# Performance work log

Hardware: AMD Instinct MI355X
Metric: run time of the kernel (lower is better)

Reference implementation:

```python
import jax, jax.numpy as jnp
import numpy as np

BUCKET_SIZE = 128
CAUSAL = True
LOOK_BACKWARD = 1
LOOK_FORWARD = 0


def look_around(x, backward=LOOK_BACKWARD, forward=LOOK_FORWARD, pad_value=-1.0):
    # x: [n, buckets, bucket_size, ...]; pad along bucket dim, gather halo windows along dim 2
    nb = x.shape[1]
    pad = [(0, 0), (backward, forward)] + [(0, 0)] * (x.ndim - 2)
    p = jnp.pad(x, pad, constant_values=pad_value)
    return jnp.concatenate([p[:, i:i + nb] for i in range(forward + backward + 1)], axis=2)


def setup_inputs() -> dict:
    key = jax.random.key(0)
    kq, kk, kv = jax.random.split(key, 3)
    shape = (4, 16, 8192, 64)  # [batch, heads, seq, head_dim]
    return {
        "q": jax.random.normal(kq, shape, jnp.float32),
        "k": jax.random.normal(kk, shape, jnp.float32),
        "v": jax.random.normal(kv, shape, jnp.float32),
    }


def reference(q, k, v):
    b, h, t, e = q.shape
    buckets = t // BUCKET_SIZE
    ticker = jnp.arange(t, dtype=q.dtype).reshape(1, buckets, BUCKET_SIZE)

    def bkt(x):
        return x.reshape(b * h, buckets, BUCKET_SIZE, e)

    bq, bk, bv = bkt(q), bkt(k), bkt(v)
    bk = look_around(bk)
    bv = look_around(bv)
    bq_t = ticker                # [1, buckets, bucket_size]
    bq_k = look_around(ticker)

    dots = jnp.einsum('nbie,nbje->nbij', bq, bk) * (e ** -0.5)
    mask_value = -jnp.finfo(dots.dtype).max
    if CAUSAL:
        causal_mask = bq_t[:, :, :, None] < bq_k[:, :, None, :]
        dots = jnp.where(causal_mask, mask_value, dots)
    pad_mask = bq_k[:, :, None, :] == -1
    dots = jnp.where(pad_mask, mask_value, dots)

    attn = jax.nn.softmax(dots, axis=-1)
    out = jnp.einsum('nbij,nbje->nbie', attn, bv)
    return out.reshape(b, h, t, e)
```

## Files before the change

### kernel.cpp

```cpp
#include <hip/hip_runtime.h>
#include <hip/hip_bf16.h>

#define T_SEQ 8192
#define E 64
#define BS 128
#define QSCALE 0.18033688f

typedef __attribute__((ext_vector_type(4))) float f32x4;
typedef __attribute__((ext_vector_type(8))) short bf16x8;

__device__ __forceinline__ float hw_exp2(float x) {
    float r;
    asm("v_exp_f32 %0, %1" : "=v"(r) : "v"(x));
    return r;
}

__device__ __forceinline__ unsigned pk2(float a, float b) {
    __hip_bfloat162 h = __float22bfloat162_rn(make_float2(a, b));
    union { __hip_bfloat162 h; unsigned u; } cv; cv.h = h;
    return cv.u;
}

union Frag { unsigned u[4]; bf16x8 v; };

__global__ __launch_bounds__(256, 2)
void la_kernel(const float* __restrict__ q, const float* __restrict__ k,
               const float* __restrict__ v, float* __restrict__ out) {
    __shared__ __align__(16) unsigned char smem[32768];
    unsigned short* KV = (unsigned short*)smem;
    float* OB = (float*)smem;

    const int raw  = blockIdx.x;
    const int work = (raw & 7) * 512 + (raw >> 3);
    const int bh = work >> 6;
    const int qb = work & 63;

    const int tid  = threadIdx.x;
    const int wv   = tid >> 6;
    const int lane = tid & 63;
    const int g    = lane >> 4;
    const int col  = lane & 15;

    const size_t base_kv = (size_t)bh * T_SEQ * E;
    const int k0 = (qb - 1) * BS;
    const int STT = (qb == 0) ? 8 : 0;
    const int SKT = (qb == 0) ? 4 : 0;

    bf16x8 qf0[2], qf1[2];
    #pragma unroll
    for (int it = 0; it < 2; ++it) {
        #pragma unroll
        for (int kq = 0; kq < 2; ++kq) {
            const float* src = q + ((size_t)bh * T_SEQ + qb * BS + wv * 32 + it * 16 + col) * E
                                 + g * 8 + kq * 32;
            float4 f0 = *(const float4*)(src);
            float4 f1 = *(const float4*)(src + 4);
            Frag fr;
            fr.u[0] = pk2(f0.x * QSCALE, f0.y * QSCALE);
            fr.u[1] = pk2(f0.z * QSCALE, f0.w * QSCALE);
            fr.u[2] = pk2(f1.x * QSCALE, f1.y * QSCALE);
            fr.u[3] = pk2(f1.z * QSCALE, f1.w * QSCALE);
            if (it) qf1[kq] = fr.v; else qf0[kq] = fr.v;
        }
    }

    {
        const int jr = tid >> 4;
        const int c4 = (tid & 15) * 4;
        #pragma unroll
        for (int t = 0; t < 16; ++t) {
            const int jj = jr + t * 16;
            const int gk = k0 + jj;
            float4 kvv = make_float4(0.f, 0.f, 0.f, 0.f);
            if (gk >= 0) kvv = *(const float4*)(k + base_kv + (size_t)gk * E + c4);
            uint2 pr;
            pr.x = pk2(kvv.x, kvv.y);
            pr.y = pk2(kvv.z, kvv.w);
            *(uint2*)(&KV[(jj * 64 + c4) ^ ((jj & 7) << 3)]) = pr;
        }
    }
    __syncthreads();

    unsigned P0[32], P1[32];
    float inv0, inv1;

    auto s_phase = [&](const int it, const bf16x8* qf, unsigned* __restrict__ P, float& inv_out) {
        const int NT = 2 * wv + it + 9;
        f32x4 S[16];
        #pragma unroll
        for (int jt = 0; jt < 16; ++jt) S[jt] = (f32x4)0.f;
        #pragma unroll
        for (int jt = 0; jt < 16; ++jt) {
            if (jt >= STT && jt < NT) {
                const int j = jt * 16 + col;
                #pragma unroll
                for (int kq = 0; kq < 2; ++kq) {
                    const int e = g * 8 + kq * 32;
                    bf16x8 kf = *(const bf16x8*)(&KV[(j * 64 + e) ^ ((j & 7) << 3)]);
                    S[jt] = __builtin_amdgcn_mfma_f32_16x16x32_bf16(kf, qf[kq], S[jt], 0, 0, 0);
                }
            }
        }
        float mx = -3.0e38f;
        #pragma unroll
        for (int jt = 0; jt < 16; ++jt) {
            if (jt >= STT && jt < NT) {
                if (jt == NT - 1) {
                    #pragma unroll
                    for (int r = 0; r < 4; ++r) {
                        float s = (4 * g + r <= col) ? S[jt][r] : -1.0e30f;
                        S[jt][r] = s;
                        mx = fmaxf(mx, s);
                    }
                } else {
                    #pragma unroll
                    for (int r = 0; r < 4; ++r) mx = fmaxf(mx, S[jt][r]);
                }
            }
        }
        mx = fmaxf(mx, __shfl_xor(mx, 16, 64));
        mx = fmaxf(mx, __shfl_xor(mx, 32, 64));
        float sum = 0.f;
        #pragma unroll
        for (int jt = 0; jt < 16; ++jt) {
            if (jt >= STT && jt < NT) {
                #pragma unroll
                for (int r = 0; r < 4; ++r) {
                    float p = hw_exp2(S[jt][r] - mx);
                    S[jt][r] = p;
                    sum += p;
                }
            }
        }
        sum += __shfl_xor(sum, 16, 64);
        sum += __shfl_xor(sum, 32, 64);
        inv_out = 1.0f / sum;
        const int NKT = wv + 5;
        #pragma unroll
        for (int kt = 0; kt < 8; ++kt) {
            if (kt >= SKT && kt < NKT) {
                P[4*kt+0] = pk2(S[2*kt  ][0], S[2*kt  ][1]);
                P[4*kt+1] = pk2(S[2*kt  ][2], S[2*kt  ][3]);
                P[4*kt+2] = pk2(S[2*kt+1][0], S[2*kt+1][1]);
                P[4*kt+3] = pk2(S[2*kt+1][2], S[2*kt+1][3]);
            } else {
                P[4*kt+0] = 0u; P[4*kt+1] = 0u; P[4*kt+2] = 0u; P[4*kt+3] = 0u;
            }
        }
    };
    s_phase(0, qf0, P0, inv0);
    s_phase(1, qf1, P1, inv1);
    __syncthreads();

    {
        const int d0 = (tid >> 4) * 4;
        const int pb = tid & 15;
        #pragma unroll
        for (int t = 0; t < 8; ++t) {
            const int p  = pb + 16 * t;
            const int gk = k0 + 2 * p;
            float4 a = make_float4(0.f,0.f,0.f,0.f), b = make_float4(0.f,0.f,0.f,0.f);
            if (gk >= 0) {
                a = *(const float4*)(v + base_kv + (size_t)gk * E + d0);
                b = *(const float4*)(v + base_kv + (size_t)(gk + 1) * E + d0);
            }
            const int jp = 2 * p;
            *(unsigned*)(&KV[((d0    ) * 256 + jp) ^ (((d0    ) & 7) << 3)]) = pk2(a.x, b.x);
            *(unsigned*)(&KV[((d0 + 1) * 256 + jp) ^ (((d0 + 1) & 7) << 3)]) = pk2(a.y, b.y);
            *(unsigned*)(&KV[((d0 + 2) * 256 + jp) ^ (((d0 + 2) & 7) << 3)]) = pk2(a.z, b.z);
            *(unsigned*)(&KV[((d0 + 3) * 256 + jp) ^ (((d0 + 3) & 7) << 3)]) = pk2(a.w, b.w);
        }
    }
    __syncthreads();

    auto pv_phase = [&](const unsigned* __restrict__ P, f32x4* __restrict__ O) {
        #pragma unroll
        for (int dt = 0; dt < 4; ++dt) O[dt] = (f32x4)0.f;
        const int s0 = ((g & 1) << 5) + col;
        const int s1 = s0 + 16;
        const bool hiSel = (g >= 2);
        const int NKT = wv + 5;
        #pragma unroll
        for (int kt = 0; kt < 8; ++kt) {
            if (kt >= SKT && kt < NKT) {
                const unsigned x0 = P[4*kt+0], x1 = P[4*kt+1], y0 = P[4*kt+2], y1 = P[4*kt+3];
                unsigned t0x = (unsigned)__shfl((int)x0, s0, 64), t0y = (unsigned)__shfl((int)y0, s0, 64);
                unsigned t1x = (unsigned)__shfl((int)x1, s0, 64), t1y = (unsigned)__shfl((int)y1, s0, 64);
                unsigned t2x = (unsigned)__shfl((int)x0, s1, 64), t2y = (unsigned)__shfl((int)y0, s1, 64);
                unsigned t3x = (unsigned)__shfl((int)x1, s1, 64), t3y = (unsigned)__shfl((int)y1, s1, 64);
                Frag af;
                af.u[0] = hiSel ? t0y : t0x;
                af.u[1] = hiSel ? t1y : t1x;
                af.u[2] = hiSel ? t2y : t2x;
                af.u[3] = hiSel ? t3y : t3x;
                const int j0 = kt * 32 + g * 8;
                #pragma unroll
                for (int dt = 0; dt < 4; ++dt) {
                    const int d = dt * 16 + col;
                    bf16x8 vf = *(const bf16x8*)(&KV[(d * 256 + j0) ^ ((d & 7) << 3)]);
                    O[dt] = __builtin_amdgcn_mfma_f32_16x16x32_bf16(af.v, vf, O[dt], 0, 0, 0);
                }
            }
        }
    };
    f32x4 O0[4], O1[4];
    pv_phase(P0, O0);
    pv_phase(P1, O1);
    __syncthreads();

    const int srcbase = (lane & 48) | ((4 * (lane >> 4)) & 15);
    float w0[4], w1[4];
    #pragma unroll
    for (int r = 0; r < 4; ++r) {
        w0[r] = __shfl(inv0, srcbase + r, 64);
        w1[r] = __shfl(inv1, srcbase + r, 64);
    }

    #pragma unroll
    for (int it2 = 0; it2 < 2; ++it2) {
        const f32x4* O = it2 ? O1 : O0;
        const float* w = it2 ? w1 : w0;
        #pragma unroll
        for (int dt = 0; dt < 4; ++dt) {
            #pragma unroll
            for (int r = 0; r < 4; ++r) {
                const int row = wv * 32 + it2 * 16 + g * 4 + r;
                const int d = dt * 16 + col;
                OB[(row * 64 + d) ^ ((row & 7) << 2)] = O[dt][r] * w[r];
            }
        }
    }
    __syncthreads();
    {
        #pragma unroll
        for (int t = 0; t < 8; ++t) {
            const int f4  = t * 256 + tid;
            const int row = f4 >> 4;
            const int c4  = (f4 & 15) * 4;
            float4 val = *(const float4*)(&OB[(row * 64 + c4) ^ ((row & 7) << 2)]);
            *(float4*)(out + ((size_t)bh * T_SEQ + qb * BS + row) * E + c4) = val;
        }
    }
}

extern "C" void kernel_launch(void* const* d_in, const int* in_sizes, int n_in,
                              void* d_out, int out_size, void* d_ws, size_t ws_size,
                              hipStream_t stream) {
    const float* q = (const float*)d_in[0];
    const float* k = (const float*)d_in[1];
    const float* v = (const float*)d_in[2];
    float* out = (float*)d_out;
    la_kernel<<<dim3(64 * 64), dim3(256), 0, stream>>>(q, k, v, out);
}
```

Baseline: 157.3 us.

## Split each query bucket into two 64-row half-blocks per workgroup

```diff
diff --git a/kernel.cpp b/kernel.cpp
--- a/kernel.cpp
+++ b/kernel.cpp
@@ -3,7 +3,6 @@
 
 #define T_SEQ 8192
 #define E 64
-#define BS 128
 #define QSCALE 0.18033688f
 
 typedef __attribute__((ext_vector_type(4))) float f32x4;
@@ -31,9 +30,11 @@
     float* OB = (float*)smem;
 
     const int raw  = blockIdx.x;
-    const int work = (raw & 7) * 512 + (raw >> 3);
-    const int bh = work >> 6;
-    const int qb = work & 63;
+    const int work = (raw & 7) * 1024 + (raw >> 3);
+    const int bh = work >> 7;
+    const int qs = work & 127;
+    const int h  = qs & 1;
+    const int qb = qs >> 1;
 
     const int tid  = threadIdx.x;
     const int wv   = tid >> 6;
@@ -42,33 +43,33 @@
     const int col  = lane & 15;
 
     const size_t base_kv = (size_t)bh * T_SEQ * E;
-    const int k0 = (qb - 1) * BS;
+    const int k0 = qb * 128 - 128;
+    const int KROWS_T = 12 + 4 * h;
+    const int VPAIR_T = 6 + 2 * h;
     const int STT = (qb == 0) ? 8 : 0;
     const int SKT = (qb == 0) ? 4 : 0;
-
-    bf16x8 qf0[2], qf1[2];
-    #pragma unroll
-    for (int it = 0; it < 2; ++it) {
-        #pragma unroll
-        for (int kq = 0; kq < 2; ++kq) {
-            const float* src = q + ((size_t)bh * T_SEQ + qb * BS + wv * 32 + it * 16 + col) * E
-                                 + g * 8 + kq * 32;
-            float4 f0 = *(const float4*)(src);
-            float4 f1 = *(const float4*)(src + 4);
-            Frag fr;
-            fr.u[0] = pk2(f0.x * QSCALE, f0.y * QSCALE);
-            fr.u[1] = pk2(f0.z * QSCALE, f0.w * QSCALE);
-            fr.u[2] = pk2(f1.x * QSCALE, f1.y * QSCALE);
-            fr.u[3] = pk2(f1.z * QSCALE, f1.w * QSCALE);
-            if (it) qf1[kq] = fr.v; else qf0[kq] = fr.v;
-        }
+    const int NT  = 9 + 4 * h + wv;
+    const int NKT = (NT + 1) >> 1;
+
+    bf16x8 qf[2];
+    #pragma unroll
+    for (int kq = 0; kq < 2; ++kq) {
+        const float* src = q + ((size_t)bh * T_SEQ + qs * 64 + wv * 16 + col) * E
+                             + g * 8 + kq * 32;
+        float4 f0 = *(const float4*)(src);
+        float4 f1 = *(const float4*)(src + 4);
+        Frag fr;
+        fr.u[0] = pk2(f0.x * QSCALE, f0.y * QSCALE);
+        fr.u[1] = pk2(f0.z * QSCALE, f0.w * QSCALE);
+        fr.u[2] = pk2(f1.x * QSCALE, f1.y * QSCALE);
+        fr.u[3] = pk2(f1.z * QSCALE, f1.w * QSCALE);
+        qf[kq] = fr.v;
     }
 
     {
         const int jr = tid >> 4;
         const int c4 = (tid & 15) * 4;
-        #pragma unroll
-        for (int t = 0; t < 16; ++t) {
+        for (int t = 0; t < KROWS_T; ++t) {
             const int jj = jr + t * 16;
             const int gk = k0 + jj;
             float4 kvv = make_float4(0.f, 0.f, 0.f, 0.f);
@@ -81,11 +82,9 @@
     }
     __syncthreads();
 
-    unsigned P0[32], P1[32];
-    float inv0, inv1;
-
-    auto s_phase = [&](const int it, const bf16x8* qf, unsigned* __restrict__ P, float& inv_out) {
-        const int NT = 2 * wv + it + 9;
+    unsigned P[32];
+    float inv;
+    {
         f32x4 S[16];
         #pragma unroll
         for (int jt = 0; jt < 16; ++jt) S[jt] = (f32x4)0.f;
@@ -134,8 +133,7 @@
         }
         sum += __shfl_xor(sum, 16, 64);
         sum += __shfl_xor(sum, 32, 64);
-        inv_out = 1.0f / sum;
-        const int NKT = wv + 5;
+        inv = 1.0f / sum;
         #pragma unroll
         for (int kt = 0; kt < 8; ++kt) {
             if (kt >= SKT && kt < NKT) {
@@ -147,16 +145,13 @@
                 P[4*kt+0] = 0u; P[4*kt+1] = 0u; P[4*kt+2] = 0u; P[4*kt+3] = 0u;
             }
         }
-    };
-    s_phase(0, qf0, P0, inv0);
-    s_phase(1, qf1, P1, inv1);
+    }
     __syncthreads();
 
     {
         const int d0 = (tid >> 4) * 4;
         const int pb = tid & 15;
-        #pragma unroll
-        for (int t = 0; t < 8; ++t) {
+        for (int t = 0; t < VPAIR_T; ++t) {
             const int p  = pb + 16 * t;
             const int gk = k0 + 2 * p;
             float4 a = make_float4(0.f,0.f,0.f,0.f), b = make_float4(0.f,0.f,0.f,0.f);
@@ -173,13 +168,13 @@
     }
     __syncthreads();
 
-    auto pv_phase = [&](const unsigned* __restrict__ P, f32x4* __restrict__ O) {
-        #pragma unroll
-        for (int dt = 0; dt < 4; ++dt) O[dt] = (f32x4)0.f;
+    f32x4 O[4];
+    #pragma unroll
+    for (int dt = 0; dt < 4; ++dt) O[dt] = (f32x4)0.f;
+    {
         const int s0 = ((g & 1) << 5) + col;
         const int s1 = s0 + 16;
         const bool hiSel = (g >= 2);
-        const int NKT = wv + 5;
         #pragma unroll
         for (int kt = 0; kt < 8; ++kt) {
             if (kt >= SKT && kt < NKT) {
@@ -202,43 +197,32 @@
                 }
             }
         }
-    };
-    f32x4 O0[4], O1[4];
-    pv_phase(P0, O0);
-    pv_phase(P1, O1);
+    }
     __syncthreads();
 
     const int srcbase = (lane & 48) | ((4 * (lane >> 4)) & 15);
-    float w0[4], w1[4];
-    #pragma unroll
-    for (int r = 0; r < 4; ++r) {
-        w0[r] = __shfl(inv0, srcbase + r, 64);
-        w1[r] = __shfl(inv1, srcbase + r, 64);
-    }
-
-    #pragma unroll
-    for (int it2 = 0; it2 < 2; ++it2) {
-        const f32x4* O = it2 ? O1 : O0;
-        const float* w = it2 ? w1 : w0;
-        #pragma unroll
-        for (int dt = 0; dt < 4; ++dt) {
-            #pragma unroll
-            for (int r = 0; r < 4; ++r) {
-                const int row = wv * 32 + it2 * 16 + g * 4 + r;
-                const int d = dt * 16 + col;
-                OB[(row * 64 + d) ^ ((row & 7) << 2)] = O[dt][r] * w[r];
-            }
-        }
-    }
-    __syncthreads();
-    {
-        #pragma unroll
-        for (int t = 0; t < 8; ++t) {
+    float w0[4];
+    #pragma unroll
+    for (int r = 0; r < 4; ++r) w0[r] = __shfl(inv, srcbase + r, 64);
+
+    #pragma unroll
+    for (int dt = 0; dt < 4; ++dt) {
+        #pragma unroll
+        for (int r = 0; r < 4; ++r) {
+            const int row = wv * 16 + g * 4 + r;
+            const int d = dt * 16 + col;
+            OB[(row * 64 + d) ^ ((row & 7) << 2)] = O[dt][r] * w0[r];
+        }
+    }
+    __syncthreads();
+    {
+        #pragma unroll
+        for (int t = 0; t < 4; ++t) {
             const int f4  = t * 256 + tid;
             const int row = f4 >> 4;
             const int c4  = (f4 & 15) * 4;
             float4 val = *(const float4*)(&OB[(row * 64 + c4) ^ ((row & 7) << 2)]);
-            *(float4*)(out + ((size_t)bh * T_SEQ + qb * BS + row) * E + c4) = val;
+            *(float4*)(out + ((size_t)bh * T_SEQ + qs * 64 + row) * E + c4) = val;
         }
     }
 }
@@ -250,5 +234,5 @@
     const float* k = (const float*)d_in[1];
     const float* v = (const float*)d_in[2];
     float* out = (float*)d_out;
-    la_kernel<<<dim3(64 * 64), dim3(256), 0, stream>>>(q, k, v, out);
-}
+    la_kernel<<<dim3(64 * 128), dim3(256), 0, stream>>>(q, k, v, out);
+}
```

New measurement: 219.1 us. +39.3%, slower.

## Process eight consecutive query buckets per block with K/V halo reuse and prefetch

Applied to the files above, without the earlier changes.

```diff
diff --git a/kernel.cpp b/kernel.cpp
--- a/kernel.cpp
+++ b/kernel.cpp
@@ -3,7 +3,7 @@
 
 #define T_SEQ 8192
 #define E 64
-#define BS 128
+#define NB 8
 #define QSCALE 0.18033688f
 
 typedef __attribute__((ext_vector_type(4))) float f32x4;
@@ -14,232 +14,291 @@
     asm("v_exp_f32 %0, %1" : "=v"(r) : "v"(x));
     return r;
 }
-
 __device__ __forceinline__ unsigned pk2(float a, float b) {
     __hip_bfloat162 h = __float22bfloat162_rn(make_float2(a, b));
     union { __hip_bfloat162 h; unsigned u; } cv; cv.h = h;
     return cv.u;
 }
-
 union Frag { unsigned u[4]; bf16x8 v; };
 
 __global__ __launch_bounds__(256, 2)
 void la_kernel(const float* __restrict__ q, const float* __restrict__ k,
                const float* __restrict__ v, float* __restrict__ out) {
-    __shared__ __align__(16) unsigned char smem[32768];
-    unsigned short* KV = (unsigned short*)smem;
-    float* OB = (float*)smem;
-
-    const int raw  = blockIdx.x;
-    const int work = (raw & 7) * 512 + (raw >> 3);
-    const int bh = work >> 6;
-    const int qb = work & 63;
+    __shared__ __align__(16) unsigned char smem[65536];
+    unsigned short* Kb = (unsigned short*)smem;
+    unsigned short* Vb = (unsigned short*)(smem + 32768);
+
+    const int w  = blockIdx.x;
+    const int bh = w >> 3;
+    const int b0 = (w & 7) * NB;
 
     const int tid  = threadIdx.x;
     const int wv   = tid >> 6;
     const int lane = tid & 63;
     const int g    = lane >> 4;
     const int col  = lane & 15;
-
-    const size_t base_kv = (size_t)bh * T_SEQ * E;
-    const int k0 = (qb - 1) * BS;
-    const int STT = (qb == 0) ? 8 : 0;
-    const int SKT = (qb == 0) ? 4 : 0;
+    const size_t base = (size_t)bh * T_SEQ * E;
+
+    const int jr  = tid >> 4;
+    const int c4  = (tid & 15) * 4;
+    const int d0v = (tid >> 4) * 4;
+    const int pbv = tid & 15;
 
     bf16x8 qf0[2], qf1[2];
     #pragma unroll
-    for (int it = 0; it < 2; ++it) {
-        #pragma unroll
-        for (int kq = 0; kq < 2; ++kq) {
-            const float* src = q + ((size_t)bh * T_SEQ + qb * BS + wv * 32 + it * 16 + col) * E
-                                 + g * 8 + kq * 32;
-            float4 f0 = *(const float4*)(src);
-            float4 f1 = *(const float4*)(src + 4);
-            Frag fr;
-            fr.u[0] = pk2(f0.x * QSCALE, f0.y * QSCALE);
-            fr.u[1] = pk2(f0.z * QSCALE, f0.w * QSCALE);
-            fr.u[2] = pk2(f1.x * QSCALE, f1.y * QSCALE);
-            fr.u[3] = pk2(f1.z * QSCALE, f1.w * QSCALE);
-            if (it) qf1[kq] = fr.v; else qf0[kq] = fr.v;
-        }
+    for (int it = 0; it < 2; ++it)
+    #pragma unroll
+    for (int kq = 0; kq < 2; ++kq) {
+        const float* src = q + base + (size_t)(b0 * 128 + wv * 32 + it * 16 + col) * E
+                             + g * 8 + kq * 32;
+        float4 f0 = *(const float4*)src, f1 = *(const float4*)(src + 4);
+        Frag fr;
+        fr.u[0] = pk2(f0.x * QSCALE, f0.y * QSCALE);
+        fr.u[1] = pk2(f0.z * QSCALE, f0.w * QSCALE);
+        fr.u[2] = pk2(f1.x * QSCALE, f1.y * QSCALE);
+        fr.u[3] = pk2(f1.z * QSCALE, f1.w * QSCALE);
+        if (it) qf1[kq] = fr.v; else qf0[kq] = fr.v;
     }
 
     {
-        const int jr = tid >> 4;
-        const int c4 = (tid & 15) * 4;
+        const int kbase = b0 * 128 - 128;
         #pragma unroll
         for (int t = 0; t < 16; ++t) {
-            const int jj = jr + t * 16;
-            const int gk = k0 + jj;
-            float4 kvv = make_float4(0.f, 0.f, 0.f, 0.f);
-            if (gk >= 0) kvv = *(const float4*)(k + base_kv + (size_t)gk * E + c4);
-            uint2 pr;
-            pr.x = pk2(kvv.x, kvv.y);
-            pr.y = pk2(kvv.z, kvv.w);
-            *(uint2*)(&KV[(jj * 64 + c4) ^ ((jj & 7) << 3)]) = pr;
+            const int jj = jr + t * 16, gk = kbase + jj;
+            float4 kv = make_float4(0.f, 0.f, 0.f, 0.f);
+            if (gk >= 0) kv = *(const float4*)(k + base + (size_t)gk * E + c4);
+            uint2 pr; pr.x = pk2(kv.x, kv.y); pr.y = pk2(kv.z, kv.w);
+            *(uint2*)(&Kb[((jj * 64 + c4) ^ ((jj & 7) << 3)) ^ 8192]) = pr;
+        }
+        #pragma unroll
+        for (int t = 0; t < 8; ++t) {
+            const int p = pbv + 16 * t, gk = kbase + 2 * p;
+            float4 a = make_float4(0,0,0,0), bb = make_float4(0,0,0,0);
+            if (gk >= 0) {
+                a  = *(const float4*)(v + base + (size_t)gk * E + d0v);
+                bb = *(const float4*)(v + base + (size_t)(gk + 1) * E + d0v);
+            }
+            const int jp = 2 * p;
+            *(unsigned*)(&Vb[(((d0v    ) * 256 + jp) ^ (((d0v    ) & 7) << 3)) ^ 128]) = pk2(a.x, bb.x);
+            *(unsigned*)(&Vb[(((d0v + 1) * 256 + jp) ^ (((d0v + 1) & 7) << 3)) ^ 128]) = pk2(a.y, bb.y);
+            *(unsigned*)(&Vb[(((d0v + 2) * 256 + jp) ^ (((d0v + 2) & 7) << 3)) ^ 128]) = pk2(a.z, bb.z);
+            *(unsigned*)(&Vb[(((d0v + 3) * 256 + jp) ^ (((d0v + 3) & 7) << 3)) ^ 128]) = pk2(a.w, bb.w);
         }
     }
     __syncthreads();
 
-    unsigned P0[32], P1[32];
-    float inv0, inv1;
-
-    auto s_phase = [&](const int it, const bf16x8* qf, unsigned* __restrict__ P, float& inv_out) {
-        const int NT = 2 * wv + it + 9;
-        f32x4 S[16];
-        #pragma unroll
-        for (int jt = 0; jt < 16; ++jt) S[jt] = (f32x4)0.f;
-        #pragma unroll
-        for (int jt = 0; jt < 16; ++jt) {
-            if (jt >= STT && jt < NT) {
-                const int j = jt * 16 + col;
-                #pragma unroll
-                for (int kq = 0; kq < 2; ++kq) {
-                    const int e = g * 8 + kq * 32;
-                    bf16x8 kf = *(const bf16x8*)(&KV[(j * 64 + e) ^ ((j & 7) << 3)]);
-                    S[jt] = __builtin_amdgcn_mfma_f32_16x16x32_bf16(kf, qf[kq], S[jt], 0, 0, 0);
-                }
-            }
-        }
-        float mx = -3.0e38f;
-        #pragma unroll
-        for (int jt = 0; jt < 16; ++jt) {
-            if (jt >= STT && jt < NT) {
-                if (jt == NT - 1) {
+    const int srcbase = (lane & 48) | ((4 * (lane >> 4)) & 15);
+
+    for (int i = 0; i < NB; ++i) {
+        const int b  = b0 + i;
+        const int px = ((b & 1) ^ 1) << 7;
+        const int kx = px << 6;
+        const int hf = px >> 7;
+        const bool last = (i == NB - 1);
+        const int STT = (b == 0) ? 8 : 0;
+        const int SKT = (b == 0) ? 4 : 0;
+
+        float4 fk[8], fva[4], fvb[4];
+        if (!last) {
+            const int kb2 = (b + 1) * 128;
+            #pragma unroll
+            for (int t = 0; t < 8; ++t)
+                fk[t] = *(const float4*)(k + base + (size_t)(kb2 + jr + 16 * t) * E + c4);
+            #pragma unroll
+            for (int t = 0; t < 4; ++t) {
+                const int p = pbv + 16 * t;
+                fva[t] = *(const float4*)(v + base + (size_t)(kb2 + 2 * p) * E + d0v);
+                fvb[t] = *(const float4*)(v + base + (size_t)(kb2 + 2 * p + 1) * E + d0v);
+            }
+        }
+
+        unsigned P0[32], P1[32];
+        float inv0, inv1;
+        auto s_phase = [&](const int it, const bf16x8* qf, unsigned* __restrict__ P, float& inv_out) {
+            const int NT = 2 * wv + it + 9;
+            f32x4 S[16];
+            #pragma unroll
+            for (int jt = 0; jt < 16; ++jt) S[jt] = (f32x4)0.f;
+            #pragma unroll
+            for (int jt = 0; jt < 16; ++jt) {
+                if (jt >= STT && jt < NT) {
+                    const int j = jt * 16 + col;
+                    #pragma unroll
+                    for (int kq = 0; kq < 2; ++kq) {
+                        const int e = g * 8 + kq * 32;
+                        bf16x8 kf = *(const bf16x8*)(&Kb[((j * 64 + e) ^ ((j & 7) << 3)) ^ kx]);
+                        S[jt] = __builtin_amdgcn_mfma_f32_16x16x32_bf16(kf, qf[kq], S[jt], 0, 0, 0);
+                    }
+                }
+            }
+            float mx = -3.0e38f;
+            #pragma unroll
+            for (int jt = 0; jt < 16; ++jt) {
+                if (jt >= STT && jt < NT) {
+                    if (jt == NT - 1) {
+                        #pragma unroll
+                        for (int r = 0; r < 4; ++r) {
+                            float s = (4 * g + r <= col) ? S[jt][r] : -1.0e30f;
+                            S[jt][r] = s;
+                            mx = fmaxf(mx, s);
+                        }
+                    } else {
+                        #pragma unroll
+                        for (int r = 0; r < 4; ++r) mx = fmaxf(mx, S[jt][r]);
+                    }
+                }
+            }
+            mx = fmaxf(mx, __shfl_xor(mx, 16, 64));
+            mx = fmaxf(mx, __shfl_xor(mx, 32, 64));
+            float sum = 0.f;
+            #pragma unroll
+            for (int jt = 0; jt < 16; ++jt) {
+                if (jt >= STT && jt < NT) {
                     #pragma unroll
                     for (int r = 0; r < 4; ++r) {
-                        float s = (4 * g + r <= col) ? S[jt][r] : -1.0e30f;
-                        S[jt][r] = s;
-                        mx = fmaxf(mx, s);
+                        float p = hw_exp2(S[jt][r] - mx);
+                        S[jt][r] = p;
+                        sum += p;
                     }
+                }
+            }
+            sum += __shfl_xor(sum, 16, 64);
+            sum += __shfl_xor(sum, 32, 64);
+            inv_out = 1.0f / sum;
+            const int NKT = wv + 5;
+            #pragma unroll
+            for (int kt = 0; kt < 8; ++kt) {
+                if (kt >= SKT && kt < NKT) {
+                    P[4*kt+0] = pk2(S[2*kt  ][0], S[2*kt  ][1]);
+                    P[4*kt+1] = pk2(S[2*kt  ][2], S[2*kt  ][3]);
+                    P[4*kt+2] = pk2(S[2*kt+1][0], S[2*kt+1][1]);
+                    P[4*kt+3] = pk2(S[2*kt+1][2], S[2*kt+1][3]);
                 } else {
+                    P[4*kt+0] = 0u; P[4*kt+1] = 0u; P[4*kt+2] = 0u; P[4*kt+3] = 0u;
+                }
+            }
+        };
+        s_phase(0, qf0, P0, inv0);
+        s_phase(1, qf1, P1, inv1);
+
+        float4 qraw[8];
+        if (!last) {
+            #pragma unroll
+            for (int it = 0; it < 2; ++it)
+            #pragma unroll
+            for (int kq = 0; kq < 2; ++kq) {
+                const float* src = q + base + (size_t)((b + 1) * 128 + wv * 32 + it * 16 + col) * E
+                                     + g * 8 + kq * 32;
+                qraw[it * 4 + kq * 2]     = *(const float4*)src;
+                qraw[it * 4 + kq * 2 + 1] = *(const float4*)(src + 4);
+            }
+        }
+
+        f32x4 O0[4], O1[4];
+        auto pv_phase = [&](const unsigned* __restrict__ P, f32x4* __restrict__ O) {
+            #pragma unroll
+            for (int dt = 0; dt < 4; ++dt) O[dt] = (f32x4)0.f;
+            const int s0 = ((g & 1) << 5) + col;
+            const int s1 = s0 + 16;
+            const bool hiSel = (g >= 2);
+            const int NKT = wv + 5;
+            #pragma unroll
+            for (int kt = 0; kt < 8; ++kt) {
+                if (kt >= SKT && kt < NKT) {
+                    const unsigned x0 = P[4*kt+0], x1 = P[4*kt+1], y0 = P[4*kt+2], y1 = P[4*kt+3];
+                    unsigned t0x = (unsigned)__shfl((int)x0, s0, 64), t0y = (unsigned)__shfl((int)y0, s0, 64);
+                    unsigned t1x = (unsigned)__shfl((int)x1, s0, 64), t1y = (unsigned)__shfl((int)y1, s0, 64);
+                    unsigned t2x = (unsigned)__shfl((int)x0, s1, 64), t2y = (unsigned)__shfl((int)y0, s1, 64);
+                    unsigned t3x = (unsigned)__shfl((int)x1, s1, 64), t3y = (unsigned)__shfl((int)y1, s1, 64);
+                    Frag af;
+                    af.u[0] = hiSel ? t0y : t0x;
+                    af.u[1] = hiSel ? t1y : t1x;
+                    af.u[2] = hiSel ? t2y : t2x;
+                    af.u[3] = hiSel ? t3y : t3x;
+                    const int j0 = kt * 32 + g * 8;
                     #pragma unroll
-                    for (int r = 0; r < 4; ++r) mx = fmaxf(mx, S[jt][r]);
-                }
-            }
-        }
-        mx = fmaxf(mx, __shfl_xor(mx, 16, 64));
-        mx = fmaxf(mx, __shfl_xor(mx, 32, 64));
-        float sum = 0.f;
+                    for (int dt = 0; dt < 4; ++dt) {
+                        const int d = dt * 16 + col;
+                        bf16x8 vf = *(const bf16x8*)(&Vb[((d * 256 + j0) ^ ((d & 7) << 3)) ^ px]);
+                        O[dt] = __builtin_amdgcn_mfma_f32_16x16x32_bf16(af.v, vf, O[dt], 0, 0, 0);
+                    }
+                }
+            }
+        };
+        pv_phase(P0, O0);
+        pv_phase(P1, O1);
+        __syncthreads();
+
+        float* FK = (float*)(smem + hf * 16384);
+        float* FV = (float*)(smem + 32768 + hf * 256);
+        float w0[4], w1[4];
         #pragma unroll
-        for (int jt = 0; jt < 16; ++jt) {
-            if (jt >= STT && jt < NT) {
+        for (int r = 0; r < 4; ++r) {
+            w0[r] = __shfl(inv0, srcbase + r, 64);
+            w1[r] = __shfl(inv1, srcbase + r, 64);
+        }
+        #pragma unroll
+        for (int it2 = 0; it2 < 2; ++it2) {
+            const f32x4* O = it2 ? O1 : O0;
+            const float* ww = it2 ? w1 : w0;
+            #pragma unroll
+            for (int dt = 0; dt < 4; ++dt) {
                 #pragma unroll
                 for (int r = 0; r < 4; ++r) {
-                    float p = hw_exp2(S[jt][r] - mx);
-                    S[jt][r] = p;
-                    sum += p;
-                }
-            }
-        }
-        sum += __shfl_xor(sum, 16, 64);
-        sum += __shfl_xor(sum, 32, 64);
-        inv_out = 1.0f / sum;
-        const int NKT = wv + 5;
-        #pragma unroll
-        for (int kt = 0; kt < 8; ++kt) {
-            if (kt >= SKT && kt < NKT) {
-                P[4*kt+0] = pk2(S[2*kt  ][0], S[2*kt  ][1]);
-                P[4*kt+1] = pk2(S[2*kt  ][2], S[2*kt  ][3]);
-                P[4*kt+2] = pk2(S[2*kt+1][0], S[2*kt+1][1]);
-                P[4*kt+3] = pk2(S[2*kt+1][2], S[2*kt+1][3]);
-            } else {
-                P[4*kt+0] = 0u; P[4*kt+1] = 0u; P[4*kt+2] = 0u; P[4*kt+3] = 0u;
-            }
-        }
-    };
-    s_phase(0, qf0, P0, inv0);
-    s_phase(1, qf1, P1, inv1);
-    __syncthreads();
-
-    {
-        const int d0 = (tid >> 4) * 4;
-        const int pb = tid & 15;
-        #pragma unroll
-        for (int t = 0; t < 8; ++t) {
-            const int p  = pb + 16 * t;
-            const int gk = k0 + 2 * p;
-            float4 a = make_float4(0.f,0.f,0.f,0.f), b = make_float4(0.f,0.f,0.f,0.f);
-            if (gk >= 0) {
-                a = *(const float4*)(v + base_kv + (size_t)gk * E + d0);
-                b = *(const float4*)(v + base_kv + (size_t)(gk + 1) * E + d0);
-            }
-            const int jp = 2 * p;
-            *(unsigned*)(&KV[((d0    ) * 256 + jp) ^ (((d0    ) & 7) << 3)]) = pk2(a.x, b.x);
-            *(unsigned*)(&KV[((d0 + 1) * 256 + jp) ^ (((d0 + 1) & 7) << 3)]) = pk2(a.y, b.y);
-            *(unsigned*)(&KV[((d0 + 2) * 256 + jp) ^ (((d0 + 2) & 7) << 3)]) = pk2(a.z, b.z);
-            *(unsigned*)(&KV[((d0 + 3) * 256 + jp) ^ (((d0 + 3) & 7) << 3)]) = pk2(a.w, b.w);
-        }
-    }
-    __syncthreads();
-
-    auto pv_phase = [&](const unsigned* __restrict__ P, f32x4* __restrict__ O) {
-        #pragma unroll
-        for (int dt = 0; dt < 4; ++dt) O[dt] = (f32x4)0.f;
-        const int s0 = ((g & 1) << 5) + col;
-        const int s1 = s0 + 16;
-        const bool hiSel = (g >= 2);
-        const int NKT = wv + 5;
-        #pragma unroll
-        for (int kt = 0; kt < 8; ++kt) {
-            if (kt >= SKT && kt < NKT) {
-                const unsigned x0 = P[4*kt+0], x1 = P[4*kt+1], y0 = P[4*kt+2], y1 = P[4*kt+3];
-                unsigned t0x = (unsigned)__shfl((int)x0, s0, 64), t0y = (unsigned)__shfl((int)y0, s0, 64);
-                unsigned t1x = (unsigned)__shfl((int)x1, s0, 64), t1y = (unsigned)__shfl((int)y1, s0, 64);
-                unsigned t2x = (unsigned)__shfl((int)x0, s1, 64), t2y = (unsigned)__shfl((int)y0, s1, 64);
-                unsigned t3x = (unsigned)__shfl((int)x1, s1, 64), t3y = (unsigned)__shfl((int)y1, s1, 64);
-                Frag af;
-                af.u[0] = hiSel ? t0y : t0x;
-                af.u[1] = hiSel ? t1y : t1x;
-                af.u[2] = hiSel ? t2y : t2x;
-                af.u[3] = hiSel ? t3y : t3x;
-                const int j0 = kt * 32 + g * 8;
-                #pragma unroll
-                for (int dt = 0; dt < 4; ++dt) {
-                    const int d = dt * 16 + col;
-                    bf16x8 vf = *(const bf16x8*)(&KV[(d * 256 + j0) ^ ((d & 7) << 3)]);
-                    O[dt] = __builtin_amdgcn_mfma_f32_16x16x32_bf16(af.v, vf, O[dt], 0, 0, 0);
-                }
-            }
-        }
-    };
-    f32x4 O0[4], O1[4];
-    pv_phase(P0, O0);
-    pv_phase(P1, O1);
-    __syncthreads();
-
-    const int srcbase = (lane & 48) | ((4 * (lane >> 4)) & 15);
-    float w0[4], w1[4];
-    #pragma unroll
-    for (int r = 0; r < 4; ++r) {
-        w0[r] = __shfl(inv0, srcbase + r, 64);
-        w1[r] = __shfl(inv1, srcbase + r, 64);
-    }
-
-    #pragma unroll
-    for (int it2 = 0; it2 < 2; ++it2) {
-        const f32x4* O = it2 ? O1 : O0;
-        const float* w = it2 ? w1 : w0;
-        #pragma unroll
-        for (int dt = 0; dt < 4; ++dt) {
-            #pragma unroll
-            for (int r = 0; r < 4; ++r) {
-                const int row = wv * 32 + it2 * 16 + g * 4 + r;
-                const int d = dt * 16 + col;
-                OB[(row * 64 + d) ^ ((row & 7) << 2)] = O[dt][r] * w[r];
-            }
-        }
-    }
-    __syncthreads();
-    {
-        #pragma unroll
-        for (int t = 0; t < 8; ++t) {
-            const int f4  = t * 256 + tid;
-            const int row = f4 >> 4;
-            const int c4  = (f4 & 15) * 4;
-            float4 val = *(const float4*)(&OB[(row * 64 + c4) ^ ((row & 7) << 2)]);
-            *(float4*)(out + ((size_t)bh * T_SEQ + qb * BS + row) * E + c4) = val;
-        }
+                    const int row = wv * 32 + it2 * 16 + g * 4 + r;
+                    const int d   = dt * 16 + col;
+                    const int sw  = (((row >> 2) ^ row) & 3) << 4;
+                    const float val = O[dt][r] * ww[r];
+                    if (wv < 2) FK[row * 64 + (d ^ sw)] = val;
+                    else        FV[(row - 64) * 128 + (d ^ sw)] = val;
+                }
+            }
+        }
+        __syncthreads();
+        {
+            #pragma unroll
+            for (int t = 0; t < 8; ++t) {
+                const int f4  = t * 256 + tid;
+                const int row = f4 >> 4;
+                const int cc  = (f4 & 15) * 4;
+                const int sw  = (((row >> 2) ^ row) & 3) << 4;
+                float4 val;
+                if (t < 4) val = *(const float4*)(&FK[row * 64 + (cc ^ sw)]);
+                else       val = *(const float4*)(&FV[(row - 64) * 128 + (cc ^ sw)]);
+                *(float4*)(out + base + (size_t)(b * 128 + row) * E + cc) = val;
+            }
+        }
+        __syncthreads();
+
+        if (!last) {
+            #pragma unroll
+            for (int it = 0; it < 2; ++it)
+            #pragma unroll
+            for (int kq = 0; kq < 2; ++kq) {
+                float4 f0 = qraw[it * 4 + kq * 2], f1 = qraw[it * 4 + kq * 2 + 1];
+                Frag fr;
+                fr.u[0] = pk2(f0.x * QSCALE, f0.y * QSCALE);
+                fr.u[1] = pk2(f0.z * QSCALE, f0.w * QSCALE);
+                fr.u[2] = pk2(f1.x * QSCALE, f1.y * QSCALE);
+                fr.u[3] = pk2(f1.z * QSCALE, f1.w * QSCALE);
+                if (it) qf1[kq] = fr.v; else qf0[kq] = fr.v;
+            }
+            #pragma unroll
+            for (int t = 0; t < 8; ++t) {
+                const int lr = jr + 16 * t;
+                uint2 pr; pr.x = pk2(fk[t].x, fk[t].y); pr.y = pk2(fk[t].z, fk[t].w);
+                *(uint2*)(&Kb[((lr * 64 + c4) ^ ((lr & 7) << 3)) + hf * 8192]) = pr;
+            }
+            #pragma unroll
+            for (int t = 0; t < 4; ++t) {
+                const int jp = 2 * (pbv + 16 * t);
+                *(unsigned*)(&Vb[(((d0v    ) * 256 + jp) ^ (((d0v    ) & 7) << 3)) + hf * 128]) = pk2(fva[t].x, fvb[t].x);
+                *(unsigned*)(&Vb[(((d0v + 1) * 256 + jp) ^ (((d0v + 1) & 7) << 3)) + hf * 128]) = pk2(fva[t].y, fvb[t].y);
+                *(unsigned*)(&Vb[(((d0v + 2) * 256 + jp) ^ (((d0v + 2) & 7) << 3)) + hf * 128]) = pk2(fva[t].z, fvb[t].z);
+                *(unsigned*)(&Vb[(((d0v + 3) * 256 + jp) ^ (((d0v + 3) & 7) << 3)) + hf * 128]) = pk2(fva[t].w, fvb[t].w);
+            }
+        }
+        __syncthreads();
     }
 }
 
@@ -250,5 +309,5 @@
     const float* k = (const float*)d_in[1];
     const float* v = (const float*)d_in[2];
     float* out = (float*)d_out;
-    la_kernel<<<dim3(64 * 64), dim3(256), 0, stream>>>(q, k, v, out);
+    la_kernel<<<dim3(64 * 8), dim3(256), 0, stream>>>(q, k, v, out);
 }
```

Measured after the change: 321.3 us. +104.3%, slower.

## Split score phase into two halves with lazy rescale to cut registers

Applied to the files above, without the earlier changes.

```diff
diff --git a/kernel.cpp b/kernel.cpp
--- a/kernel.cpp
+++ b/kernel.cpp
@@ -3,7 +3,6 @@
 
 #define T_SEQ 8192
 #define E 64
-#define BS 128
 #define QSCALE 0.18033688f
 
 typedef __attribute__((ext_vector_type(4))) float f32x4;
@@ -14,16 +13,20 @@
     asm("v_exp_f32 %0, %1" : "=v"(r) : "v"(x));
     return r;
 }
-
 __device__ __forceinline__ unsigned pk2(float a, float b) {
     __hip_bfloat162 h = __float22bfloat162_rn(make_float2(a, b));
     union { __hip_bfloat162 h; unsigned u; } cv; cv.h = h;
     return cv.u;
 }
-
+__device__ __forceinline__ float bf_lo(unsigned u) {
+    union { unsigned u; float f; } c; c.u = u << 16; return c.f;
+}
+__device__ __forceinline__ float bf_hi(unsigned u) {
+    union { unsigned u; float f; } c; c.u = u & 0xFFFF0000u; return c.f;
+}
 union Frag { unsigned u[4]; bf16x8 v; };
 
-__global__ __launch_bounds__(256, 2)
+__global__ __launch_bounds__(256, 4)
 void la_kernel(const float* __restrict__ q, const float* __restrict__ k,
                const float* __restrict__ v, float* __restrict__ out) {
     __shared__ __align__(16) unsigned char smem[32768];
@@ -42,7 +45,7 @@
     const int col  = lane & 15;
 
     const size_t base_kv = (size_t)bh * T_SEQ * E;
-    const int k0 = (qb - 1) * BS;
+    const int k0 = (qb - 1) * 128;
     const int STT = (qb == 0) ? 8 : 0;
     const int SKT = (qb == 0) ? 4 : 0;
 
@@ -51,7 +54,7 @@
     for (int it = 0; it < 2; ++it) {
         #pragma unroll
         for (int kq = 0; kq < 2; ++kq) {
-            const float* src = q + ((size_t)bh * T_SEQ + qb * BS + wv * 32 + it * 16 + col) * E
+            const float* src = q + ((size_t)bh * T_SEQ + qb * 128 + wv * 32 + it * 16 + col) * E
                                  + g * 8 + kq * 32;
             float4 f0 = *(const float4*)(src);
             float4 f1 = *(const float4*)(src + 4);
@@ -86,12 +89,14 @@
 
     auto s_phase = [&](const int it, const bf16x8* qf, unsigned* __restrict__ P, float& inv_out) {
         const int NT = 2 * wv + it + 9;
-        f32x4 S[16];
-        #pragma unroll
-        for (int jt = 0; jt < 16; ++jt) S[jt] = (f32x4)0.f;
-        #pragma unroll
-        for (int jt = 0; jt < 16; ++jt) {
-            if (jt >= STT && jt < NT) {
+        f32x4 S[8];
+        float mA = -3.0e38f, sA = 0.f;
+
+        if (STT == 0) {
+            #pragma unroll
+            for (int jt = 0; jt < 8; ++jt) S[jt] = (f32x4)0.f;
+            #pragma unroll
+            for (int jt = 0; jt < 8; ++jt) {
                 const int j = jt * 16 + col;
                 #pragma unroll
                 for (int kq = 0; kq < 2; ++kq) {
@@ -100,53 +105,102 @@
                     S[jt] = __builtin_amdgcn_mfma_f32_16x16x32_bf16(kf, qf[kq], S[jt], 0, 0, 0);
                 }
             }
-        }
-        float mx = -3.0e38f;
-        #pragma unroll
-        for (int jt = 0; jt < 16; ++jt) {
-            if (jt >= STT && jt < NT) {
-                if (jt == NT - 1) {
-                    #pragma unroll
-                    for (int r = 0; r < 4; ++r) {
-                        float s = (4 * g + r <= col) ? S[jt][r] : -1.0e30f;
-                        S[jt][r] = s;
-                        mx = fmaxf(mx, s);
-                    }
-                } else {
-                    #pragma unroll
-                    for (int r = 0; r < 4; ++r) mx = fmaxf(mx, S[jt][r]);
-                }
-            }
-        }
-        mx = fmaxf(mx, __shfl_xor(mx, 16, 64));
-        mx = fmaxf(mx, __shfl_xor(mx, 32, 64));
-        float sum = 0.f;
-        #pragma unroll
-        for (int jt = 0; jt < 16; ++jt) {
-            if (jt >= STT && jt < NT) {
+            #pragma unroll
+            for (int jt = 0; jt < 8; ++jt)
+                #pragma unroll
+                for (int r = 0; r < 4; ++r) mA = fmaxf(mA, S[jt][r]);
+            mA = fmaxf(mA, __shfl_xor(mA, 16, 64));
+            mA = fmaxf(mA, __shfl_xor(mA, 32, 64));
+            #pragma unroll
+            for (int jt = 0; jt < 8; ++jt) {
                 #pragma unroll
                 for (int r = 0; r < 4; ++r) {
-                    float p = hw_exp2(S[jt][r] - mx);
+                    float p = hw_exp2(S[jt][r] - mA);
                     S[jt][r] = p;
-                    sum += p;
-                }
-            }
-        }
-        sum += __shfl_xor(sum, 16, 64);
-        sum += __shfl_xor(sum, 32, 64);
-        inv_out = 1.0f / sum;
-        const int NKT = wv + 5;
-        #pragma unroll
-        for (int kt = 0; kt < 8; ++kt) {
-            if (kt >= SKT && kt < NKT) {
+                    sA += p;
+                }
+            }
+            #pragma unroll
+            for (int kt = 0; kt < 4; ++kt) {
                 P[4*kt+0] = pk2(S[2*kt  ][0], S[2*kt  ][1]);
                 P[4*kt+1] = pk2(S[2*kt  ][2], S[2*kt  ][3]);
                 P[4*kt+2] = pk2(S[2*kt+1][0], S[2*kt+1][1]);
                 P[4*kt+3] = pk2(S[2*kt+1][2], S[2*kt+1][3]);
-            } else {
-                P[4*kt+0] = 0u; P[4*kt+1] = 0u; P[4*kt+2] = 0u; P[4*kt+3] = 0u;
-            }
-        }
+            }
+        } else {
+            #pragma unroll
+            for (int i2 = 0; i2 < 16; ++i2) P[i2] = 0u;
+        }
+
+        float mB = -3.0e38f, sB = 0.f;
+        #pragma unroll
+        for (int jt8 = 0; jt8 < 8; ++jt8) S[jt8] = (f32x4)0.f;
+        #pragma unroll
+        for (int jt8 = 0; jt8 < 8; ++jt8) {
+            const int jt = 8 + jt8;
+            if (jt < NT) {
+                const int j = jt * 16 + col;
+                #pragma unroll
+                for (int kq = 0; kq < 2; ++kq) {
+                    const int e = g * 8 + kq * 32;
+                    bf16x8 kf = *(const bf16x8*)(&KV[(j * 64 + e) ^ ((j & 7) << 3)]);
+                    S[jt8] = __builtin_amdgcn_mfma_f32_16x16x32_bf16(kf, qf[kq], S[jt8], 0, 0, 0);
+                }
+            }
+        }
+        #pragma unroll
+        for (int jt8 = 0; jt8 < 8; ++jt8) {
+            const int jt = 8 + jt8;
+            if (jt < NT) {
+                if (jt == NT - 1) {
+                    #pragma unroll
+                    for (int r = 0; r < 4; ++r) {
+                        float s = (4 * g + r <= col) ? S[jt8][r] : -1.0e30f;
+                        S[jt8][r] = s;
+                        mB = fmaxf(mB, s);
+                    }
+                } else {
+                    #pragma unroll
+                    for (int r = 0; r < 4; ++r) mB = fmaxf(mB, S[jt8][r]);
+                }
+            }
+        }
+        mB = fmaxf(mB, __shfl_xor(mB, 16, 64));
+        mB = fmaxf(mB, __shfl_xor(mB, 32, 64));
+        const float m = (mB <= mA + 8.f) ? mA : mB;
+        #pragma unroll
+        for (int jt8 = 0; jt8 < 8; ++jt8) {
+            const int jt = 8 + jt8;
+            if (jt < NT) {
+                #pragma unroll
+                for (int r = 0; r < 4; ++r) {
+                    float p = hw_exp2(S[jt8][r] - m);
+                    S[jt8][r] = p;
+                    sB += p;
+                }
+            }
+        }
+        #pragma unroll
+        for (int kt8 = 0; kt8 < 4; ++kt8) {
+            P[16+4*kt8+0] = pk2(S[2*kt8  ][0], S[2*kt8  ][1]);
+            P[16+4*kt8+1] = pk2(S[2*kt8  ][2], S[2*kt8  ][3]);
+            P[16+4*kt8+2] = pk2(S[2*kt8+1][0], S[2*kt8+1][1]);
+            P[16+4*kt8+3] = pk2(S[2*kt8+1][2], S[2*kt8+1][3]);
+        }
+        if (__any(mB > mA + 8.f)) {
+            const float scaleA = hw_exp2(mA - m);
+            #pragma unroll
+            for (int i2 = 0; i2 < 16; ++i2) {
+                float a = bf_lo(P[i2]) * scaleA;
+                float b = bf_hi(P[i2]) * scaleA;
+                P[i2] = pk2(a, b);
+            }
+            sA *= scaleA;
+        }
+        float sum = sA + sB;
+        sum += __shfl_xor(sum, 16, 64);
+        sum += __shfl_xor(sum, 32, 64);
+        inv_out = 1.0f / sum;
     };
     s_phase(0, qf0, P0, inv0);
     s_phase(1, qf1, P1, inv1);
@@ -238,7 +292,7 @@
             const int row = f4 >> 4;
             const int c4  = (f4 & 15) * 4;
             float4 val = *(const float4*)(&OB[(row * 64 + c4) ^ ((row & 7) << 2)]);
-            *(float4*)(out + ((size_t)bh * T_SEQ + qb * BS + row) * E + c4) = val;
+            *(float4*)(out + ((size_t)bh * T_SEQ + qb * 128 + row) * E + c4) = val;
         }
     }
 }
```

Result: faster. 143.5 us (-8.8%).
